# Optimization experiments

Measured on AMD Instinct MI355X. Metric: run time of the kernel, lower is better.

The kernel has to match this reference:

```python
import jax, jax.numpy as jnp
import numpy as np

B, L, LC, C, H = 4, 1024, 1024, 1024, 16
HD = C // H
SCALE = 0.25 / (HD ** 0.5)
EPS = 1e-5

def _ln(x):
    mu = jnp.mean(x, axis=-1, keepdims=True)
    var = jnp.mean(jnp.square(x - mu), axis=-1, keepdims=True)
    return (x - mu) * jax.lax.rsqrt(var + EPS)

def setup_inputs() -> dict:
    key = jax.random.key(0)
    ks = jax.random.split(key, 16)
    s = 0.02
    return {
        'x': jax.random.normal(ks[0], (B, L, C), jnp.float32),
        'context': jax.random.normal(ks[1], (B, LC, C), jnp.float32),
        'cond_BD': jax.random.normal(ks[2], (B, 1, 6, C), jnp.float32),
        'attn_bias': jax.random.normal(ks[3], (B, H, L, LC), jnp.float32) * 0.1,
        'ada_gss': jax.random.normal(ks[4], (1, 1, 6, C), jnp.float32) / (C ** 0.5),
        'Wq': jax.random.normal(ks[5], (C, C), jnp.float32) * s,
        'Wk': jax.random.normal(ks[6], (C, C), jnp.float32) * s,
        'Wv': jax.random.normal(ks[7], (C, C), jnp.float32) * s,
        'Wo': jax.random.normal(ks[8], (C, C), jnp.float32) * s,
        'bo': jnp.zeros((C,), jnp.float32),
        'W1': jax.random.normal(ks[9], (4 * C, C), jnp.float32) * s,
        'b1': jnp.zeros((4 * C,), jnp.float32),
        'W2': jax.random.normal(ks[10], (C, 4 * C), jnp.float32) * s,
        'b2': jnp.zeros((C,), jnp.float32),
    }

def reference(x, context, cond_BD, attn_bias, ada_gss, Wq, Wk, Wv, Wo, bo, W1, b1, W2, b2):
    # AdaLN params: [B,1,6,C] -> six [B,1,C] tensors
    g = ada_gss + cond_BD
    gamma1, gamma2, scale1, scale2, shift1, shift2 = [g[:, :, i] for i in range(6)]

    # --- cross attention branch ---
    mod_x = _ln(x) * (scale1 + 1.0) + shift1  # [B,L,C]
    q = jnp.einsum('blc,dc->bld', mod_x, Wq).reshape(B, L, H, HD).transpose(0, 2, 1, 3)
    k = jnp.einsum('bmc,dc->bmd', context, Wk).reshape(B, LC, H, HD).transpose(0, 2, 1, 3)
    v = jnp.einsum('bmc,dc->bmd', context, Wv).reshape(B, LC, H, HD).transpose(0, 2, 1, 3)
    attn = jnp.einsum('bhld,bhmd->bhlm', q, k) * SCALE + attn_bias
    attn = jax.nn.softmax(attn, axis=-1)
    out = jnp.einsum('bhlm,bhmd->bhld', attn, v).transpose(0, 2, 1, 3).reshape(B, L, C)
    attn_out = jnp.einsum('blc,dc->bld', out, Wo) + bo
    x = x + attn_out * gamma1

    # --- FFN branch ---
    mod_f = _ln(x) * (scale2 + 1.0) + shift2
    h = jax.nn.gelu(jnp.einsum('blc,hc->blh', mod_f, W1) + b1, approximate=True)
    ffn_out = jnp.einsum('blh,ch->blc', h, W2) + b2
    return x + ffn_out * gamma2
```

## Files before the change

kernel.cpp:

```cpp
#include <hip/hip_runtime.h>

typedef _Float16 half8 __attribute__((ext_vector_type(8)));
typedef _Float16 half4v __attribute__((ext_vector_type(4)));
typedef float f32x4 __attribute__((ext_vector_type(4)));

#define MFMA16(a, b, c) __builtin_amdgcn_mfma_f32_16x16x32_f16((a), (b), (c), 0, 0, 0)

__device__ __forceinline__ void gl2lds16(const void* g, void* l) {
  __builtin_amdgcn_global_load_lds(
      (const __attribute__((address_space(1))) void*)g,
      (__attribute__((address_space(3))) void*)l, 16, 0, 0);
}

__global__ void cast_f16_kernel(const float* __restrict__ in, _Float16* __restrict__ out, int n) {
  int i = (blockIdx.x * 256 + threadIdx.x) * 8;
  if (i >= n) return;
  float4 a = *(const float4*)(in + i);
  float4 b = *(const float4*)(in + i + 4);
  half8 o;
  o[0] = (_Float16)a.x; o[1] = (_Float16)a.y; o[2] = (_Float16)a.z; o[3] = (_Float16)a.w;
  o[4] = (_Float16)b.x; o[5] = (_Float16)b.y; o[6] = (_Float16)b.z; o[7] = (_Float16)b.w;
  *(half8*)(out + i) = o;
}

__global__ void ln_mod_kernel(const float* __restrict__ x, const float* __restrict__ cond,
                              const float* __restrict__ ada, _Float16* __restrict__ out,
                              int sidx, int hidx) {
  int row = blockIdx.x;
  int b = row >> 10;
  int t = threadIdx.x;
  const float* xr = x + (size_t)row * 1024;
  float4 v = *(const float4*)(xr + t * 4);
  float s = v.x + v.y + v.z + v.w;
  float s2 = v.x * v.x + v.y * v.y + v.z * v.z + v.w * v.w;
#pragma unroll
  for (int m = 32; m >= 1; m >>= 1) {
    s += __shfl_xor(s, m, 64);
    s2 += __shfl_xor(s2, m, 64);
  }
  __shared__ float red[8];
  int w = t >> 6;
  if ((t & 63) == 0) { red[w * 2] = s; red[w * 2 + 1] = s2; }
  __syncthreads();
  s = red[0] + red[2] + red[4] + red[6];
  s2 = red[1] + red[3] + red[5] + red[7];
  float mu = s * (1.f / 1024.f);
  float var = s2 * (1.f / 1024.f) - mu * mu;
  float rstd = rsqrtf(var + 1e-5f);
  int c = t * 4;
  float4 sc = *(const float4*)(cond + (size_t)b * 6144 + sidx * 1024 + c);
  float4 sh = *(const float4*)(cond + (size_t)b * 6144 + hidx * 1024 + c);
  float4 sa = *(const float4*)(ada + sidx * 1024 + c);
  float4 ha = *(const float4*)(ada + hidx * 1024 + c);
  half4v o;
  o[0] = (_Float16)((v.x - mu) * rstd * (sc.x + sa.x + 1.f) + sh.x + ha.x);
  o[1] = (_Float16)((v.y - mu) * rstd * (sc.y + sa.y + 1.f) + sh.y + ha.y);
  o[2] = (_Float16)((v.z - mu) * rstd * (sc.z + sa.z + 1.f) + sh.z + ha.z);
  o[3] = (_Float16)((v.w - mu) * rstd * (sc.w + sa.w + 1.f) + sh.w + ha.w);
  *(half4v*)(out + (size_t)row * 1024 + c) = o;
}

template <int EPI>
__global__ __launch_bounds__(256) void gemm_f16(
    const _Float16* __restrict__ A, const _Float16* __restrict__ W,
    int M, int N, int K, void* __restrict__ outp,
    const float* __restrict__ bias, const float* __restrict__ res,
    const float* __restrict__ cond, const float* __restrict__ ada, int gidx) {
  __shared__ __align__(16) _Float16 lA[128 * 32];
  __shared__ __align__(16) _Float16 lB[128 * 32];
  int t = threadIdx.x;
  int lane = t & 63;
  int w = t >> 6;
  int wr = w >> 1, wc = w & 1;
  int l16 = lane & 15, lg = lane >> 4;
  int bm = blockIdx.y * 128, bn = blockIdx.x * 128;
  f32x4 acc[4][4] = {};
  int e0 = t * 8;
  int e1 = 2048 + t * 8;
  int r0 = e0 >> 5, c0 = e0 & 31;
  int r1 = e1 >> 5, c1 = e1 & 31;
  const _Float16* Ab = A + (size_t)bm * K;
  const _Float16* Wb = W + (size_t)bn * K;
  for (int kt = 0; kt < K; kt += 32) {
    gl2lds16(Ab + (size_t)r0 * K + kt + c0, &lA[e0]);
    gl2lds16(Ab + (size_t)r1 * K + kt + c1, &lA[e1]);
    gl2lds16(Wb + (size_t)r0 * K + kt + c0, &lB[e0]);
    gl2lds16(Wb + (size_t)r1 * K + kt + c1, &lB[e1]);
    __syncthreads();
    half8 af[4], bf[4];
#pragma unroll
    for (int m = 0; m < 4; ++m)
      af[m] = *(const half8*)&lA[(wr * 64 + m * 16 + l16) * 32 + lg * 8];
#pragma unroll
    for (int n = 0; n < 4; ++n)
      bf[n] = *(const half8*)&lB[(wc * 64 + n * 16 + l16) * 32 + lg * 8];
#pragma unroll
    for (int m = 0; m < 4; ++m)
#pragma unroll
      for (int n = 0; n < 4; ++n)
        acc[m][n] = MFMA16(af[m], bf[n], acc[m][n]);
    __syncthreads();
  }
#pragma unroll
  for (int m = 0; m < 4; ++m) {
#pragma unroll
    for (int n = 0; n < 4; ++n) {
      int gc = bn + wc * 64 + n * 16 + l16;
      int gr0 = bm + wr * 64 + m * 16 + lg * 4;
#pragma unroll
      for (int r = 0; r < 4; ++r) {
        int gr = gr0 + r;
        float v = acc[m][n][r];
        if constexpr (EPI == 0) {
          int b = gr >> 10, l = gr & 1023, h = gc >> 6, hd = gc & 63;
          ((_Float16*)outp)[(((size_t)(b * 16 + h)) * 1024 + l) * 64 + hd] = (_Float16)v;
        } else if constexpr (EPI == 1) {
          float g = ada[gidx * 1024 + gc] + cond[(size_t)(gr >> 10) * 6144 + gidx * 1024 + gc];
          ((float*)outp)[(size_t)gr * 1024 + gc] =
              res[(size_t)gr * 1024 + gc] + (v + bias[gc]) * g;
        } else {
          float xx = v + bias[gc];
          float u = 0.7978845608028654f * (xx + 0.044715f * xx * xx * xx);
          float e = __expf(2.f * u);
          float th = (e - 1.f) / (e + 1.f);
          ((_Float16*)outp)[(size_t)gr * 4096 + gc] = (_Float16)(0.5f * xx * (1.f + th));
        }
      }
    }
  }
}

__global__ void transpose_v_kernel(const _Float16* __restrict__ v16, _Float16* __restrict__ vt16) {
  int bh = blockIdx.y, ktile = blockIdx.x;
  __shared__ _Float16 tile[64][72];
  int t = threadIdx.x;
  int r = t >> 2, c0 = (t & 3) * 16;
  const _Float16* src = v16 + ((size_t)bh * 1024 + ktile * 64) * 64;
  half8 a = *(const half8*)(src + r * 64 + c0);
  half8 b = *(const half8*)(src + r * 64 + c0 + 8);
#pragma unroll
  for (int j = 0; j < 8; ++j) {
    tile[r][c0 + j] = a[j];
    tile[r][c0 + 8 + j] = b[j];
  }
  __syncthreads();
  half8 oa, ob;
#pragma unroll
  for (int j = 0; j < 8; ++j) {
    oa[j] = tile[c0 + j][r];
    ob[j] = tile[c0 + 8 + j][r];
  }
  _Float16* dst = vt16 + ((size_t)bh * 64 + r) * 1024 + ktile * 64 + c0;
  *(half8*)dst = oa;
  *(half8*)(dst + 8) = ob;
}

__global__ __launch_bounds__(256) void attn_kernel(
    const _Float16* __restrict__ q16, const _Float16* __restrict__ k16,
    const _Float16* __restrict__ vt16, const float* __restrict__ bias,
    _Float16* __restrict__ o16) {
  int bh = blockIdx.y;
  int qb = blockIdx.x;
  int t = threadIdx.x, w = t >> 6, lane = t & 63;
  int l16 = lane & 15, lg = lane >> 4;
  int qRowW = qb * 64 + w * 16;
  const size_t bhoff = (size_t)bh * 1024 * 64;
  half8 aq[2];
#pragma unroll
  for (int ks = 0; ks < 2; ++ks)
    aq[ks] = *(const half8*)(q16 + bhoff + (size_t)(qRowW + l16) * 64 + ks * 32 + lg * 8);
  f32x4 oacc[4] = {};
  float mrun[4], lrun[4];
#pragma unroll
  for (int r = 0; r < 4; ++r) { mrun[r] = -1e30f; lrun[r] = 0.f; }
  __shared__ __align__(16) _Float16 pbuf[4][16 * 64];
  const float* bb = bias + (size_t)bh * 1024 * 1024;
  const _Float16* vb = vt16 + (size_t)bh * 64 * 1024;
  for (int kt = 0; kt < 1024; kt += 64) {
    f32x4 s[4] = {};
#pragma unroll
    for (int ks = 0; ks < 2; ++ks) {
#pragma unroll
      for (int n = 0; n < 4; ++n) {
        half8 bk = *(const half8*)(k16 + bhoff + (size_t)(kt + n * 16 + l16) * 64 + ks * 32 + lg * 8);
        s[n] = MFMA16(aq[ks], bk, s[n]);
      }
    }
    float p[4][4];
#pragma unroll
    for (int r = 0; r < 4; ++r) {
      const float* bp = bb + (size_t)(qRowW + lg * 4 + r) * 1024 + kt + l16;
#pragma unroll
      for (int n = 0; n < 4; ++n)
        p[n][r] = s[n][r] * 0.03125f + bp[n * 16];
    }
#pragma unroll
    for (int r = 0; r < 4; ++r) {
      float tm = fmaxf(fmaxf(p[0][r], p[1][r]), fmaxf(p[2][r], p[3][r]));
#pragma unroll
      for (int msk = 1; msk < 16; msk <<= 1) tm = fmaxf(tm, __shfl_xor(tm, msk, 64));
      float mnew = fmaxf(mrun[r], tm);
      float scl = __expf(mrun[r] - mnew);
      mrun[r] = mnew;
      float ts = 0.f;
#pragma unroll
      for (int n = 0; n < 4; ++n) {
        p[n][r] = __expf(p[n][r] - mnew);
        ts += p[n][r];
      }
#pragma unroll
      for (int msk = 1; msk < 16; msk <<= 1) ts += __shfl_xor(ts, msk, 64);
      lrun[r] = lrun[r] * scl + ts;
#pragma unroll
      for (int n = 0; n < 4; ++n) {
        oacc[n][r] *= scl;
        pbuf[w][(lg * 4 + r) * 64 + n * 16 + l16] = (_Float16)p[n][r];
      }
    }
#pragma unroll
    for (int ks = 0; ks < 2; ++ks) {
      half8 ap = *(const half8*)&pbuf[w][l16 * 64 + ks * 32 + lg * 8];
#pragma unroll
      for (int n = 0; n < 4; ++n) {
        half8 bv = *(const half8*)(vb + (size_t)(n * 16 + l16) * 1024 + kt + ks * 32 + lg * 8);
        oacc[n] = MFMA16(ap, bv, oacc[n]);
      }
    }
  }
  int b = bh >> 4, h = bh & 15;
#pragma unroll
  for (int r = 0; r < 4; ++r) {
    float inv = 1.f / lrun[r];
    int row = qRowW + lg * 4 + r;
#pragma unroll
    for (int n = 0; n < 4; ++n)
      o16[((size_t)b * 1024 + row) * 1024 + h * 64 + n * 16 + l16] =
          (_Float16)(oacc[n][r] * inv);
  }
}

extern "C" void kernel_launch(void* const* d_in, const int* in_sizes, int n_in,
                              void* d_out, int out_size, void* d_ws, size_t ws_size,
                              hipStream_t stream) {
  const float* x = (const float*)d_in[0];
  const float* ctx = (const float*)d_in[1];
  const float* cond = (const float*)d_in[2];
  const float* bias = (const float*)d_in[3];
  const float* ada = (const float*)d_in[4];
  const float* Wq = (const float*)d_in[5];
  const float* Wk = (const float*)d_in[6];
  const float* Wv = (const float*)d_in[7];
  const float* Wo = (const float*)d_in[8];
  const float* bo = (const float*)d_in[9];
  const float* W1 = (const float*)d_in[10];
  const float* b1 = (const float*)d_in[11];
  const float* W2 = (const float*)d_in[12];
  const float* b2 = (const float*)d_in[13];

  char* ws = (char*)d_ws;
  const size_t MB = 1u << 20;
  _Float16* wq16 = (_Float16*)(ws + 0 * MB);
  _Float16* wk16 = (_Float16*)(ws + 2 * MB);
  _Float16* wv16 = (_Float16*)(ws + 4 * MB);
  _Float16* wo16 = (_Float16*)(ws + 6 * MB);
  _Float16* w116 = (_Float16*)(ws + 8 * MB);
  _Float16* w216 = (_Float16*)(ws + 16 * MB);
  _Float16* modx = (_Float16*)(ws + 24 * MB);
  _Float16* ctx16 = (_Float16*)(ws + 32 * MB);
  _Float16* q16 = (_Float16*)(ws + 40 * MB);
  _Float16* k16 = (_Float16*)(ws + 48 * MB);
  _Float16* v16 = (_Float16*)(ws + 56 * MB);
  _Float16* vt16 = (_Float16*)(ws + 64 * MB);
  _Float16* h16 = (_Float16*)(ws + 40 * MB);
  _Float16* o16 = (_Float16*)(ws + 72 * MB);
  float* x1 = (float*)(ws + 80 * MB);

  cast_f16_kernel<<<2048, 256, 0, stream>>>(ctx, ctx16, 4 * 1024 * 1024);
  cast_f16_kernel<<<512, 256, 0, stream>>>(Wq, wq16, 1024 * 1024);
  cast_f16_kernel<<<512, 256, 0, stream>>>(Wk, wk16, 1024 * 1024);
  cast_f16_kernel<<<512, 256, 0, stream>>>(Wv, wv16, 1024 * 1024);
  cast_f16_kernel<<<512, 256, 0, stream>>>(Wo, wo16, 1024 * 1024);
  cast_f16_kernel<<<2048, 256, 0, stream>>>(W1, w116, 4 * 1024 * 1024);
  cast_f16_kernel<<<2048, 256, 0, stream>>>(W2, w216, 4 * 1024 * 1024);

  ln_mod_kernel<<<4096, 256, 0, stream>>>(x, cond, ada, modx, 2, 4);

  dim3 gN1024(8, 32);
  gemm_f16<0><<<gN1024, 256, 0, stream>>>(modx, wq16, 4096, 1024, 1024, q16,
                                          nullptr, nullptr, nullptr, nullptr, 0);
  gemm_f16<0><<<gN1024, 256, 0, stream>>>(ctx16, wk16, 4096, 1024, 1024, k16,
                                          nullptr, nullptr, nullptr, nullptr, 0);
  gemm_f16<0><<<gN1024, 256, 0, stream>>>(ctx16, wv16, 4096, 1024, 1024, v16,
                                          nullptr, nullptr, nullptr, nullptr, 0);

  transpose_v_kernel<<<dim3(16, 64), 256, 0, stream>>>(v16, vt16);

  attn_kernel<<<dim3(16, 64), 256, 0, stream>>>(q16, k16, vt16, bias, o16);

  gemm_f16<1><<<gN1024, 256, 0, stream>>>(o16, wo16, 4096, 1024, 1024, x1,
                                          bo, x, cond, ada, 0);

  ln_mod_kernel<<<4096, 256, 0, stream>>>(x1, cond, ada, modx, 3, 5);

  gemm_f16<2><<<dim3(32, 32), 256, 0, stream>>>(modx, w116, 4096, 4096, 1024, h16,
                                                b1, nullptr, nullptr, nullptr, 0);

  gemm_f16<1><<<gN1024, 256, 0, stream>>>(h16, w216, 4096, 1024, 4096, d_out,
                                          b2, x1, cond, ada, 1);
}
```

Baseline: 857.2 us.

## Restructure attention softmax with transposed scores, prefetched bias, and fuse cast kernels

The attention kernel now computes S^T (K as the A operand) so each lane owns one query row. Row-max and row-sum reductions then need only two cross-lane shuffles, and rescaling is skipped when the max does not grow. The bias tile is loaded as vectorised f32x4 and prefetched one iteration ahead, and exp uses exp2f. The P buffer in LDS is padded to cut bank conflicts, and launch bounds request 4 blocks per CU. The seven separate cast launches are merged into one kernel, trading some register pressure and shuffle overhead for fewer launches and better bias-load latency hiding.

```diff
diff --git a/kernel.cpp b/kernel.cpp
--- a/kernel.cpp
+++ b/kernel.cpp
@@ -12,15 +12,32 @@
       (__attribute__((address_space(3))) void*)l, 16, 0, 0);
 }
 
-__global__ void cast_f16_kernel(const float* __restrict__ in, _Float16* __restrict__ out, int n) {
-  int i = (blockIdx.x * 256 + threadIdx.x) * 8;
-  if (i >= n) return;
-  float4 a = *(const float4*)(in + i);
-  float4 b = *(const float4*)(in + i + 4);
+__device__ __forceinline__ void cast8(const float* s, _Float16* d, int i) {
+  float4 a = *(const float4*)(s + i);
+  float4 b = *(const float4*)(s + i + 4);
   half8 o;
   o[0] = (_Float16)a.x; o[1] = (_Float16)a.y; o[2] = (_Float16)a.z; o[3] = (_Float16)a.w;
   o[4] = (_Float16)b.x; o[5] = (_Float16)b.y; o[6] = (_Float16)b.z; o[7] = (_Float16)b.w;
-  *(half8*)(out + i) = o;
+  *(half8*)(d + i) = o;
+}
+
+__global__ void cast_all_kernel(const float* s0, const float* s1, const float* s2,
+                                const float* s3, const float* s4, const float* s5,
+                                const float* s6, _Float16* d0, _Float16* d1,
+                                _Float16* d2, _Float16* d3, _Float16* d4,
+                                _Float16* d5, _Float16* d6) {
+  int b = blockIdx.x;
+  const float* s;
+  _Float16* d;
+  int off;
+  if (b < 2048)      { s = s0; d = d0; off = b; }
+  else if (b < 2560) { s = s1; d = d1; off = b - 2048; }
+  else if (b < 3072) { s = s2; d = d2; off = b - 2560; }
+  else if (b < 3584) { s = s3; d = d3; off = b - 3072; }
+  else if (b < 4096) { s = s4; d = d4; off = b - 3584; }
+  else if (b < 6144) { s = s5; d = d5; off = b - 4096; }
+  else               { s = s6; d = d6; off = b - 6144; }
+  cast8(s, d, (off * 256 + threadIdx.x) * 8);
 }
 
 __global__ void ln_mod_kernel(const float* __restrict__ x, const float* __restrict__ cond,
@@ -155,7 +172,7 @@
   *(half8*)(dst + 8) = ob;
 }
 
-__global__ __launch_bounds__(256) void attn_kernel(
+__global__ __launch_bounds__(256, 4) void attn_kernel(
     const _Float16* __restrict__ q16, const _Float16* __restrict__ k16,
     const _Float16* __restrict__ vt16, const float* __restrict__ bias,
     _Float16* __restrict__ o16) {
@@ -164,62 +181,82 @@
   int t = threadIdx.x, w = t >> 6, lane = t & 63;
   int l16 = lane & 15, lg = lane >> 4;
   int qRowW = qb * 64 + w * 16;
-  const size_t bhoff = (size_t)bh * 1024 * 64;
+  const size_t bhoff = (size_t)bh * 65536;
   half8 aq[2];
 #pragma unroll
   for (int ks = 0; ks < 2; ++ks)
     aq[ks] = *(const half8*)(q16 + bhoff + (size_t)(qRowW + l16) * 64 + ks * 32 + lg * 8);
   f32x4 oacc[4] = {};
-  float mrun[4], lrun[4];
-#pragma unroll
-  for (int r = 0; r < 4; ++r) { mrun[r] = -1e30f; lrun[r] = 0.f; }
-  __shared__ __align__(16) _Float16 pbuf[4][16 * 64];
-  const float* bb = bias + (size_t)bh * 1024 * 1024;
-  const _Float16* vb = vt16 + (size_t)bh * 64 * 1024;
+  float mrun = -1e30f, lrun = 0.f;
+  __shared__ __align__(16) _Float16 pbuf[4][16][80];
+  const float* bb = bias + (size_t)bh * 1048576 + (size_t)(qRowW + l16) * 1024;
+  const _Float16* kb = k16 + bhoff;
+  const _Float16* vb = vt16 + bhoff;
+  f32x4 nb[4];
+#pragma unroll
+  for (int kk = 0; kk < 4; ++kk) nb[kk] = *(const f32x4*)(bb + kk * 16 + lg * 4);
   for (int kt = 0; kt < 1024; kt += 64) {
     f32x4 s[4] = {};
 #pragma unroll
     for (int ks = 0; ks < 2; ++ks) {
 #pragma unroll
-      for (int n = 0; n < 4; ++n) {
-        half8 bk = *(const half8*)(k16 + bhoff + (size_t)(kt + n * 16 + l16) * 64 + ks * 32 + lg * 8);
-        s[n] = MFMA16(aq[ks], bk, s[n]);
+      for (int kk = 0; kk < 4; ++kk) {
+        half8 kf = *(const half8*)(kb + (size_t)(kt + kk * 16 + l16) * 64 + ks * 32 + lg * 8);
+        s[kk] = MFMA16(kf, aq[ks], s[kk]);
       }
     }
     float p[4][4];
-#pragma unroll
-    for (int r = 0; r < 4; ++r) {
-      const float* bp = bb + (size_t)(qRowW + lg * 4 + r) * 1024 + kt + l16;
+    float tm = -1e30f;
+#pragma unroll
+    for (int kk = 0; kk < 4; ++kk)
+#pragma unroll
+      for (int r = 0; r < 4; ++r) {
+        p[kk][r] = s[kk][r] * 0.03125f + nb[kk][r];
+        tm = fmaxf(tm, p[kk][r]);
+      }
+    if (kt < 960) {
+#pragma unroll
+      for (int kk = 0; kk < 4; ++kk)
+        nb[kk] = *(const f32x4*)(bb + kt + 64 + kk * 16 + lg * 4);
+    }
+    tm = fmaxf(tm, __shfl_xor(tm, 16, 64));
+    tm = fmaxf(tm, __shfl_xor(tm, 32, 64));
+    int noskip = !__all(tm <= mrun);
+    float mnew = noskip ? fmaxf(mrun, tm) : mrun;
+    float ts = 0.f;
+#pragma unroll
+    for (int kk = 0; kk < 4; ++kk)
+#pragma unroll
+      for (int r = 0; r < 4; ++r) {
+        p[kk][r] = exp2f((p[kk][r] - mnew) * 1.442695041f);
+        ts += p[kk][r];
+      }
+    ts += __shfl_xor(ts, 16, 64);
+    ts += __shfl_xor(ts, 32, 64);
+    if (noskip) {
+      float scl = exp2f((mrun - mnew) * 1.442695041f);
+      lrun = lrun * scl + ts;
+      mrun = mnew;
+      float sclr[4];
+#pragma unroll
+      for (int r = 0; r < 4; ++r) sclr[r] = __shfl(scl, lg * 4 + r, 16);
 #pragma unroll
       for (int n = 0; n < 4; ++n)
-        p[n][r] = s[n][r] * 0.03125f + bp[n * 16];
-    }
-#pragma unroll
-    for (int r = 0; r < 4; ++r) {
-      float tm = fmaxf(fmaxf(p[0][r], p[1][r]), fmaxf(p[2][r], p[3][r]));
-#pragma unroll
-      for (int msk = 1; msk < 16; msk <<= 1) tm = fmaxf(tm, __shfl_xor(tm, msk, 64));
-      float mnew = fmaxf(mrun[r], tm);
-      float scl = __expf(mrun[r] - mnew);
-      mrun[r] = mnew;
-      float ts = 0.f;
-#pragma unroll
-      for (int n = 0; n < 4; ++n) {
-        p[n][r] = __expf(p[n][r] - mnew);
-        ts += p[n][r];
-      }
-#pragma unroll
-      for (int msk = 1; msk < 16; msk <<= 1) ts += __shfl_xor(ts, msk, 64);
-      lrun[r] = lrun[r] * scl + ts;
-#pragma unroll
-      for (int n = 0; n < 4; ++n) {
-        oacc[n][r] *= scl;
-        pbuf[w][(lg * 4 + r) * 64 + n * 16 + l16] = (_Float16)p[n][r];
-      }
+#pragma unroll
+        for (int r = 0; r < 4; ++r) oacc[n][r] *= sclr[r];
+    } else {
+      lrun += ts;
+    }
+#pragma unroll
+    for (int kk = 0; kk < 4; ++kk) {
+      half4v ph;
+#pragma unroll
+      for (int r = 0; r < 4; ++r) ph[r] = (_Float16)p[kk][r];
+      *(half4v*)&pbuf[w][l16][kk * 16 + lg * 4] = ph;
     }
 #pragma unroll
     for (int ks = 0; ks < 2; ++ks) {
-      half8 ap = *(const half8*)&pbuf[w][l16 * 64 + ks * 32 + lg * 8];
+      half8 ap = *(const half8*)&pbuf[w][l16][ks * 32 + lg * 8];
 #pragma unroll
       for (int n = 0; n < 4; ++n) {
         half8 bv = *(const half8*)(vb + (size_t)(n * 16 + l16) * 1024 + kt + ks * 32 + lg * 8);
@@ -227,15 +264,18 @@
       }
     }
   }
+  float inv = 1.f / lrun;
+  float invr[4];
+#pragma unroll
+  for (int r = 0; r < 4; ++r) invr[r] = __shfl(inv, lg * 4 + r, 16);
   int b = bh >> 4, h = bh & 15;
 #pragma unroll
   for (int r = 0; r < 4; ++r) {
-    float inv = 1.f / lrun[r];
     int row = qRowW + lg * 4 + r;
 #pragma unroll
     for (int n = 0; n < 4; ++n)
       o16[((size_t)b * 1024 + row) * 1024 + h * 64 + n * 16 + l16] =
-          (_Float16)(oacc[n][r] * inv);
+          (_Float16)(oacc[n][r] * invr[r]);
   }
 }
 
@@ -275,13 +315,8 @@
   _Float16* o16 = (_Float16*)(ws + 72 * MB);
   float* x1 = (float*)(ws + 80 * MB);
 
-  cast_f16_kernel<<<2048, 256, 0, stream>>>(ctx, ctx16, 4 * 1024 * 1024);
-  cast_f16_kernel<<<512, 256, 0, stream>>>(Wq, wq16, 1024 * 1024);
-  cast_f16_kernel<<<512, 256, 0, stream>>>(Wk, wk16, 1024 * 1024);
-  cast_f16_kernel<<<512, 256, 0, stream>>>(Wv, wv16, 1024 * 1024);
-  cast_f16_kernel<<<512, 256, 0, stream>>>(Wo, wo16, 1024 * 1024);
-  cast_f16_kernel<<<2048, 256, 0, stream>>>(W1, w116, 4 * 1024 * 1024);
-  cast_f16_kernel<<<2048, 256, 0, stream>>>(W2, w216, 4 * 1024 * 1024);
+  cast_all_kernel<<<8192, 256, 0, stream>>>(ctx, Wq, Wk, Wv, Wo, W1, W2,
+                                            ctx16, wq16, wk16, wv16, wo16, w116, w216);
 
   ln_mod_kernel<<<4096, 256, 0, stream>>>(x, cond, ada, modx, 2, 4);
 
```

Result: no change. 849.5 us (-0.9%).
